# Optimization experiments

Measured on AMD Instinct MI355X. Metric: run time of the kernel, lower is better.

## Reference

```python
import jax, jax.numpy as jnp
import numpy as np

BASE_T = 0.07
ALPHA = 0.5
EPS = 1e-12  # torch F.normalize eps


def _l2_normalize(x):
    norm = jnp.linalg.norm(x, axis=1, keepdims=True)
    return x / jnp.maximum(norm, EPS)


def setup_inputs() -> dict:
    key = jax.random.key(0)
    k1, k2, k3 = jax.random.split(key, 3)
    B, D, H, W = 4096, 512, 16, 16
    return {
        "emb1": jax.random.normal(k1, (B, D), dtype=jnp.float32),
        "emb2": jax.random.normal(k2, (B, D), dtype=jnp.float32),
        "attention_map": jax.random.uniform(k3, (B, H, W), dtype=jnp.float32),
    }


def reference(emb1, emb2, attention_map):
    B = emb1.shape[0]
    e1 = _l2_normalize(emb1)
    e2 = _l2_normalize(emb2)

    att = attention_map.mean(axis=(1, 2))                     # [B]
    temp = (BASE_T * (1.0 + ALPHA * att))[:, None]            # [B, 1]

    x = jnp.concatenate([e1, e2], axis=0)                     # [2B, D]
    x_swap = jnp.concatenate([e2, e1], axis=0)                # [2B, D]
    temp_cat = jnp.concatenate([temp, temp], axis=0)          # [2B, 1]

    sim = jnp.matmul(x, x.T) / temp_cat                       # [2B, 2B]
    pos_sim = jnp.sum(x * x_swap, axis=1) / temp_cat[:, 0]    # [2B]

    diag = jnp.eye(2 * B, dtype=bool)
    sim = jnp.where(diag, -jnp.inf, sim)                      # exp(-inf) = 0

    denominator = jnp.exp(sim).sum(axis=1)                    # [2B]
    loss = -jnp.log(jnp.exp(pos_sim) / denominator)
    return loss.mean()
```

## Files before the change

kernel.cpp:

```cpp
#include <hip/hip_runtime.h>
#include <hip/hip_bf16.h>
#include <math.h>

#define B_ROWS 4096
#define D_DIM 512
#define TWO_B 8192
#define HW_N 256
#define BASE_T 0.07f
#define ALPHA_C 0.5f
#define LOG2E 1.44269504088896340736f

#define GSTRIDE 1056
#define ABUF (32 * GSTRIDE)

typedef float v4f __attribute__((ext_vector_type(4)));

__device__ __forceinline__ float fast_exp2(float x) {
#if __has_builtin(__builtin_amdgcn_exp2f)
    return __builtin_amdgcn_exp2f(x);
#else
    return exp2f(x);
#endif
}

__global__ __launch_bounds__(256) void prep_kernel(
    const float* __restrict__ emb1, const float* __restrict__ emb2,
    const float* __restrict__ att, unsigned short* __restrict__ X8,
    float* __restrict__ inv_temp, float* __restrict__ pos)
{
    const int b = blockIdx.x;
    const int t = threadIdx.x;
    const float2 a1 = ((const float2*)(emb1 + (size_t)b * D_DIM))[t];
    const float2 a2 = ((const float2*)(emb2 + (size_t)b * D_DIM))[t];
    float av = att[(size_t)b * HW_N + t];
    float s1  = a1.x * a1.x + a1.y * a1.y;
    float s2  = a2.x * a2.x + a2.y * a2.y;
    float s12 = a1.x * a2.x + a1.y * a2.y;
    #pragma unroll
    for (int m = 1; m < 64; m <<= 1) {
        s1  += __shfl_xor(s1, m, 64);
        s2  += __shfl_xor(s2, m, 64);
        s12 += __shfl_xor(s12, m, 64);
        av  += __shfl_xor(av, m, 64);
    }
    __shared__ float red[4][4];
    const int w = t >> 6, lane = t & 63;
    if (lane == 0) { red[w][0] = s1; red[w][1] = s2; red[w][2] = s12; red[w][3] = av; }
    __syncthreads();
    const float T1  = red[0][0] + red[1][0] + red[2][0] + red[3][0];
    const float T2  = red[0][1] + red[1][1] + red[2][1] + red[3][1];
    const float T12 = red[0][2] + red[1][2] + red[2][2] + red[3][2];
    const float Ta  = red[0][3] + red[1][3] + red[2][3] + red[3][3];
    const float i1 = 1.0f / fmaxf(sqrtf(T1), 1e-12f);
    const float i2 = 1.0f / fmaxf(sqrtf(T2), 1e-12f);
    const float it = 1.0f / (BASE_T * (1.0f + ALPHA_C * (Ta * (1.0f / 256.0f))));
    const int p1 = __builtin_amdgcn_cvt_pk_fp8_f32(a1.x * i1, a1.y * i1, 0, false);
    const int p2 = __builtin_amdgcn_cvt_pk_fp8_f32(a2.x * i2, a2.y * i2, 0, false);
    X8[(size_t)b * 256 + t]            = (unsigned short)(p1 & 0xffff);
    X8[(size_t)(b + B_ROWS) * 256 + t] = (unsigned short)(p2 & 0xffff);
    if (t == 0) {
        inv_temp[b] = it * LOG2E;
        inv_temp[b + B_ROWS] = it * LOG2E;
        pos[b] = (T12 * i1 * i2) * it;
    }
}

__device__ __forceinline__ void gload_lds16(const void* g, void* s) {
    __builtin_amdgcn_global_load_lds(
        (const __attribute__((address_space(1))) unsigned int*)g,
        (__attribute__((address_space(3))) unsigned int*)s,
        16, 0, 0);
}

__global__ __launch_bounds__(256) void gram_kernel(
    const unsigned char* __restrict__ X8,
    const float* __restrict__ inv_temp,
    float* __restrict__ partial)
{
    extern __shared__ unsigned char sm[];

    const int bid = (blockIdx.x & 7) * 260 + (blockIdx.x >> 3);
    int rb = (int)((129.0f - sqrtf(129.0f * 129.0f - 8.0f * (float)bid)) * 0.5f);
    rb = rb < 0 ? 0 : (rb > 63 ? 63 : rb);
    while (rb > 0 && (rb * (129 - rb)) / 2 > bid) rb--;
    while (rb < 63 && ((rb + 1) * (129 - (rb + 1))) / 2 <= bid) rb++;
    const int cb = rb + (bid - (rb * (129 - rb)) / 2);

    const int rowBase = rb * 128;
    const int colBase = cb * 128;

    const int tid  = threadIdx.x;
    const int w    = tid >> 6;
    const int lane = tid & 63;
    const int quad = lane >> 4;
    const int t    = lane & 15;
    const int wm   = w >> 1;
    const int wn   = w & 1;

    const int srow   = lane >> 4;
    const int schunk = lane & 15;

    const unsigned char* Arow0 = X8 + (size_t)rowBase * D_DIM;
    const unsigned char* Brow0 = X8 + (size_t)colBase * D_DIM;

    v4f acc[4][4];
    #pragma unroll
    for (int a = 0; a < 4; a++)
        #pragma unroll
        for (int b2 = 0; b2 < 4; b2++)
            acc[a][b2] = v4f{0.0f, 0.0f, 0.0f, 0.0f};

    int aOff[4], bOff[4];
    #pragma unroll
    for (int mi = 0; mi < 4; mi++)
        aOff[mi] = (wm * 16 + mi * 4 + (t >> 2)) * GSTRIDE + (t & 3) * 256;
    #pragma unroll
    for (int ni = 0; ni < 4; ni++)
        bOff[ni] = ABUF + (wn * 16 + ni * 4 + (t >> 2)) * GSTRIDE + (t & 3) * 256;

    for (int p = 0; p < 2; p++) {
        const int kk = p * 256;
        #pragma unroll
        for (int j = 0; j < 8; j++) {
            const int g = w * 8 + j;
            const int r = g * 4 + srow;
            gload_lds16(Arow0 + (size_t)r * D_DIM + kk + schunk * 16,
                        &sm[g * GSTRIDE]);
            gload_lds16(Brow0 + (size_t)r * D_DIM + kk + schunk * 16,
                        &sm[ABUF + g * GSTRIDE]);
        }
        __syncthreads();

        #pragma unroll
        for (int s = 0; s < 8; s++) {
            const int off = s * 32 + quad * 8;
            long aF[4], bF[4];
            #pragma unroll
            for (int mi = 0; mi < 4; mi++)
                aF[mi] = *(const long*)&sm[aOff[mi] + off];
            #pragma unroll
            for (int ni = 0; ni < 4; ni++)
                bF[ni] = *(const long*)&sm[bOff[ni] + off];
            #pragma unroll
            for (int mi = 0; mi < 4; mi++)
                #pragma unroll
                for (int ni = 0; ni < 4; ni++)
                    acc[mi][ni] = __builtin_amdgcn_mfma_f32_16x16x32_fp8_fp8(
                        aF[mi], bF[ni], acc[mi][ni], 0, 0, 0);
        }
        if (p == 0) __syncthreads();
    }

    v4f itv[4];
    #pragma unroll
    for (int mi = 0; mi < 4; mi++)
        itv[mi] = *(const v4f*)&inv_temp[rowBase + wm * 64 + mi * 16 + quad * 4];

    float* prow = partial + (size_t)(cb * 2 + wn) * TWO_B;
    #pragma unroll
    for (int mi = 0; mi < 4; mi++) {
        #pragma unroll
        for (int r = 0; r < 4; r++) {
            const int i = rowBase + wm * 64 + mi * 16 + quad * 4 + r;
            const float it = itv[mi][r];
            float s = 0.0f;
            #pragma unroll
            for (int ni = 0; ni < 4; ni++) {
                const int j = colBase + wn * 64 + ni * 16 + t;
                const float v = fast_exp2(acc[mi][ni][r] * it);
                s += (i == j) ? 0.0f : v;
            }
            s += __shfl_xor(s, 1, 64);
            s += __shfl_xor(s, 2, 64);
            s += __shfl_xor(s, 4, 64);
            s += __shfl_xor(s, 8, 64);
            if (t == 0) prow[i] = s;
        }
    }

    if (rb != cb) {
        float itj[4];
        float cs[4] = {0.0f, 0.0f, 0.0f, 0.0f};
        #pragma unroll
        for (int ni = 0; ni < 4; ni++)
            itj[ni] = inv_temp[colBase + wn * 64 + ni * 16 + t];
        #pragma unroll
        for (int mi = 0; mi < 4; mi++)
            #pragma unroll
            for (int r = 0; r < 4; r++)
                #pragma unroll
                for (int ni = 0; ni < 4; ni++)
                    cs[ni] += fast_exp2(acc[mi][ni][r] * itj[ni]);
        float* pcol = partial + (size_t)(rb * 2 + wm) * TWO_B;
        #pragma unroll
        for (int ni = 0; ni < 4; ni++) {
            cs[ni] += __shfl_xor(cs[ni], 16, 64);
            cs[ni] += __shfl_xor(cs[ni], 32, 64);
            if (quad == 0) pcol[colBase + wn * 64 + ni * 16 + t] = cs[ni];
        }
    }
}

__global__ __launch_bounds__(256) void finish1(
    const float* __restrict__ partial, const float* __restrict__ pos,
    float* __restrict__ blockSums)
{
    const int i = blockIdx.x * 256 + threadIdx.x;
    float d = 0.0f;
    #pragma unroll 8
    for (int s = 0; s < 128; s++) d += partial[(size_t)s * TWO_B + i];
    float li = logf(d) - pos[i & (B_ROWS - 1)];
    #pragma unroll
    for (int m = 1; m < 64; m <<= 1) li += __shfl_xor(li, m, 64);
    __shared__ float red[4];
    const int w = threadIdx.x >> 6, lane = threadIdx.x & 63;
    if (lane == 0) red[w] = li;
    __syncthreads();
    if (threadIdx.x == 0) blockSums[blockIdx.x] = red[0] + red[1] + red[2] + red[3];
}

__global__ void finish2(const float* __restrict__ blockSums, float* __restrict__ out)
{
    const int lane = threadIdx.x;
    float v = (lane < 32) ? blockSums[lane] : 0.0f;
    #pragma unroll
    for (int m = 1; m < 64; m <<= 1) v += __shfl_xor(v, m, 64);
    if (lane == 0) out[0] = v * (1.0f / 8192.0f);
}

extern "C" void kernel_launch(void* const* d_in, const int* in_sizes, int n_in,
                              void* d_out, int out_size, void* d_ws, size_t ws_size,
                              hipStream_t stream) {
    const float* emb1 = (const float*)d_in[0];
    const float* emb2 = (const float*)d_in[1];
    const float* att  = (const float*)d_in[2];
    float* out = (float*)d_out;

    char* ws = (char*)d_ws;
    unsigned short* X8 = (unsigned short*)ws;
    float* inv_temp    = (float*)(ws + 4194304);
    float* pos         = (float*)(ws + 4227072);
    float* partial     = (float*)(ws + 4243456);
    float* blockSums   = (float*)(ws + 8437760);

    static bool attr_set = false;
    if (!attr_set) {
        hipFuncSetAttribute((const void*)gram_kernel,
                            hipFuncAttributeMaxDynamicSharedMemorySize, 2 * ABUF);
        attr_set = true;
    }

    prep_kernel<<<B_ROWS, 256, 0, stream>>>(emb1, emb2, att, X8, inv_temp, pos);
    gram_kernel<<<2080, 256, 2 * ABUF, stream>>>((const unsigned char*)X8,
                                                 inv_temp, partial);
    finish1<<<TWO_B / 256, 256, 0, stream>>>(partial, pos, blockSums);
    finish2<<<1, 64, 0, stream>>>(blockSums, out);
}
```

Baseline: 142.8 us.

## Split K across two wave groups in gram kernel with XOR-swizzled LDS

The gram kernel now runs 512 threads per block and loads the whole 128x512 A and B tiles into 128KB of LDS in a single phase. Two groups of four waves each handle one half of K, then combine their partial accumulators through LDS. The LDS padding is replaced by an XOR swizzle of 16-byte chunks to avoid bank conflicts. finish1 moves to 64-thread blocks to use more blocks and drop its shared-memory reduction. The change trades more LDS per block (occupancy drops to one block per CU) and an extra LDS reduction for more waves sharing each tile and one fewer barrier phase.

```diff
diff --git a/kernel.cpp b/kernel.cpp
--- a/kernel.cpp
+++ b/kernel.cpp
@@ -9,9 +9,6 @@
 #define BASE_T 0.07f
 #define ALPHA_C 0.5f
 #define LOG2E 1.44269504088896340736f
-
-#define GSTRIDE 1056
-#define ABUF (32 * GSTRIDE)
 
 typedef float v4f __attribute__((ext_vector_type(4)));
 
@@ -72,7 +69,7 @@
         16, 0, 0);
 }
 
-__global__ __launch_bounds__(256) void gram_kernel(
+__global__ __launch_bounds__(512, 1) void gram_kernel(
     const unsigned char* __restrict__ X8,
     const float* __restrict__ inv_temp,
     float* __restrict__ partial)
@@ -91,11 +88,13 @@
 
     const int tid  = threadIdx.x;
     const int w    = tid >> 6;
+    const int kg   = w >> 2;
+    const int ws   = w & 3;
     const int lane = tid & 63;
     const int quad = lane >> 4;
     const int t    = lane & 15;
-    const int wm   = w >> 1;
-    const int wn   = w & 1;
+    const int wm   = ws >> 1;
+    const int wn   = ws & 1;
 
     const int srow   = lane >> 4;
     const int schunk = lane & 15;
@@ -110,46 +109,61 @@
         for (int b2 = 0; b2 < 4; b2++)
             acc[a][b2] = v4f{0.0f, 0.0f, 0.0f, 0.0f};
 
-    int aOff[4], bOff[4];
+    #pragma unroll
+    for (int j = 0; j < 16; j++) {
+        const int g2  = w * 16 + j;
+        const int buf = g2 >> 5;
+        const int rg  = g2 & 31;
+        const int r   = rg * 4 + srow;
+        const int gc  = schunk ^ (r & 15);
+        const unsigned char* base = (buf & 2) ? Brow0 : Arow0;
+        const int khalf = (buf & 1) * 256;
+        gload_lds16(base + (size_t)r * D_DIM + khalf + gc * 16,
+                    &sm[buf * 32768 + rg * 1024]);
+    }
+    __syncthreads();
+
+    const unsigned char* bA = sm + kg * 32768;
+    const unsigned char* bB = sm + 65536 + kg * 32768;
+    #pragma unroll
+    for (int s = 0; s < 8; s++) {
+        const int pu = (s * 2 + (quad >> 1)) ^ t;
+        const int off = pu * 16 + (quad & 1) * 8;
+        long aF[4], bF[4];
+        #pragma unroll
+        for (int mi = 0; mi < 4; mi++)
+            aF[mi] = *(const long*)&bA[(wm * 64 + mi * 16 + t) * 256 + off];
+        #pragma unroll
+        for (int ni = 0; ni < 4; ni++)
+            bF[ni] = *(const long*)&bB[(wn * 64 + ni * 16 + t) * 256 + off];
+        #pragma unroll
+        for (int mi = 0; mi < 4; mi++)
+            #pragma unroll
+            for (int ni = 0; ni < 4; ni++)
+                acc[mi][ni] = __builtin_amdgcn_mfma_f32_16x16x32_fp8_fp8(
+                    aF[mi], bF[ni], acc[mi][ni], 0, 0, 0);
+    }
+
+    __syncthreads();
+    if (kg == 1) {
+        #pragma unroll
+        for (int mi = 0; mi < 4; mi++)
+            #pragma unroll
+            for (int ni = 0; ni < 4; ni++)
+                *(v4f*)&sm[ws * 16384 + (((mi * 4 + ni) * 64) + lane) * 16] =
+                    acc[mi][ni];
+    }
+    __syncthreads();
+    if (kg == 1) return;
+
     #pragma unroll
     for (int mi = 0; mi < 4; mi++)
-        aOff[mi] = (wm * 16 + mi * 4 + (t >> 2)) * GSTRIDE + (t & 3) * 256;
-    #pragma unroll
-    for (int ni = 0; ni < 4; ni++)
-        bOff[ni] = ABUF + (wn * 16 + ni * 4 + (t >> 2)) * GSTRIDE + (t & 3) * 256;
-
-    for (int p = 0; p < 2; p++) {
-        const int kk = p * 256;
-        #pragma unroll
-        for (int j = 0; j < 8; j++) {
-            const int g = w * 8 + j;
-            const int r = g * 4 + srow;
-            gload_lds16(Arow0 + (size_t)r * D_DIM + kk + schunk * 16,
-                        &sm[g * GSTRIDE]);
-            gload_lds16(Brow0 + (size_t)r * D_DIM + kk + schunk * 16,
-                        &sm[ABUF + g * GSTRIDE]);
+        #pragma unroll
+        for (int ni = 0; ni < 4; ni++) {
+            const v4f o = *(const v4f*)
+                &sm[ws * 16384 + (((mi * 4 + ni) * 64) + lane) * 16];
+            acc[mi][ni] = acc[mi][ni] + o;
         }
-        __syncthreads();
-
-        #pragma unroll
-        for (int s = 0; s < 8; s++) {
-            const int off = s * 32 + quad * 8;
-            long aF[4], bF[4];
-            #pragma unroll
-            for (int mi = 0; mi < 4; mi++)
-                aF[mi] = *(const long*)&sm[aOff[mi] + off];
-            #pragma unroll
-            for (int ni = 0; ni < 4; ni++)
-                bF[ni] = *(const long*)&sm[bOff[ni] + off];
-            #pragma unroll
-            for (int mi = 0; mi < 4; mi++)
-                #pragma unroll
-                for (int ni = 0; ni < 4; ni++)
-                    acc[mi][ni] = __builtin_amdgcn_mfma_f32_16x16x32_fp8_fp8(
-                        aF[mi], bF[ni], acc[mi][ni], 0, 0, 0);
-        }
-        if (p == 0) __syncthreads();
-    }
 
     v4f itv[4];
     #pragma unroll
@@ -201,28 +215,24 @@
     }
 }
 
-__global__ __launch_bounds__(256) void finish1(
+__global__ __launch_bounds__(64) void finish1(
     const float* __restrict__ partial, const float* __restrict__ pos,
     float* __restrict__ blockSums)
 {
-    const int i = blockIdx.x * 256 + threadIdx.x;
+    const int i = blockIdx.x * 64 + threadIdx.x;
     float d = 0.0f;
     #pragma unroll 8
     for (int s = 0; s < 128; s++) d += partial[(size_t)s * TWO_B + i];
     float li = logf(d) - pos[i & (B_ROWS - 1)];
     #pragma unroll
     for (int m = 1; m < 64; m <<= 1) li += __shfl_xor(li, m, 64);
-    __shared__ float red[4];
-    const int w = threadIdx.x >> 6, lane = threadIdx.x & 63;
-    if (lane == 0) red[w] = li;
-    __syncthreads();
-    if (threadIdx.x == 0) blockSums[blockIdx.x] = red[0] + red[1] + red[2] + red[3];
+    if (threadIdx.x == 0) blockSums[blockIdx.x] = li;
 }
 
 __global__ void finish2(const float* __restrict__ blockSums, float* __restrict__ out)
 {
     const int lane = threadIdx.x;
-    float v = (lane < 32) ? blockSums[lane] : 0.0f;
+    float v = blockSums[lane] + blockSums[lane + 64];
     #pragma unroll
     for (int m = 1; m < 64; m <<= 1) v += __shfl_xor(v, m, 64);
     if (lane == 0) out[0] = v * (1.0f / 8192.0f);
@@ -246,13 +256,13 @@
     static bool attr_set = false;
     if (!attr_set) {
         hipFuncSetAttribute((const void*)gram_kernel,
-                            hipFuncAttributeMaxDynamicSharedMemorySize, 2 * ABUF);
+                            hipFuncAttributeMaxDynamicSharedMemorySize, 131072);
         attr_set = true;
     }
 
     prep_kernel<<<B_ROWS, 256, 0, stream>>>(emb1, emb2, att, X8, inv_temp, pos);
-    gram_kernel<<<2080, 256, 2 * ABUF, stream>>>((const unsigned char*)X8,
-                                                 inv_temp, partial);
-    finish1<<<TWO_B / 256, 256, 0, stream>>>(partial, pos, blockSums);
+    gram_kernel<<<2080, 512, 131072, stream>>>((const unsigned char*)X8,
+                                               inv_temp, partial);
+    finish1<<<TWO_B / 64, 64, 0, stream>>>(partial, pos, blockSums);
     finish2<<<1, 64, 0, stream>>>(blockSums, out);
 }
```

New measurement: 162.7 us. 1.14x slower.
